# Kernel optimization log

Hardware: AMD Instinct MI355X
Metric: run time of the kernel (lower is better)

Reference implementation:

```python
import jax, jax.numpy as jnp
import numpy as np

LN_ZERO = -100000000000.0
F_, D_, C_, V_ = 250000, 4, 2, 250000
E_ = F_ * D_
CD_ = C_ ** D_


def setup_inputs() -> dict:
    key = jax.random.key(0)
    k1, k2, k3 = jax.random.split(key, 3)
    # each factor has exactly D_ incident edges, one per variable slot
    edge_f = np.repeat(np.arange(E_ // D_ * 0 + F_ * 0 + F_)[:F_], D_)  # [E]
    pos = np.tile(np.arange(D_), F_)  # variable slot of each edge within its factor
    edge_v = np.asarray(jax.random.randint(k3, (E_,), 0, V_))
    # digit of each flat factor state along each axis: digits[k, s] in [0, C)
    state = np.arange(CD_)
    digits = (state[None, :] // (C_ ** (D_ - 1 - np.arange(D_)))[:, None]) % C_  # [D, CD]
    s_p = digits[pos]  # [E, CD]: the edge's own variable state within each factor state
    # permutation indices into the broadcast-first layout [E, C, C^(D-1)]
    scatter_idx = (np.arange(E_)[:, None] * CD_ + s_p * C_ ** (D_ - 1)).reshape(-1)
    fac_states_to_var = (np.arange(E_)[:, None] * C_ + s_p).reshape(-1)
    return {
        "prv_factorToVar_messages": jax.random.normal(k1, (E_, C_), jnp.float32),
        "factor_potentials": jax.random.normal(k2, (F_,) + (C_,) * D_, jnp.float32),
        "facToVar_edge_idx": jnp.asarray(np.stack([edge_f, edge_v]), jnp.int32),
        "facStates_to_varIdx": jnp.asarray(fac_states_to_var, jnp.int32),
        "varToFactorMsg_scatter_indices": jnp.asarray(scatter_idx, jnp.int32),
        "factor_potential_masks": jnp.zeros((F_,) + (C_,) * D_, jnp.int32),
        "factorToVar_messages_masks": jnp.zeros((E_, C_), bool),
        "varToFactor_messages_masks": jnp.zeros((E_, C_), bool),
        "var_beliefs_masks": jnp.zeros((V_, C_), bool),
    }


def _mask_clamp(x, mask):
    return jnp.maximum(jnp.where(mask, LN_ZERO, x), LN_ZERO)


def reference(prv_factorToVar_messages, factor_potentials, facToVar_edge_idx,
              facStates_to_varIdx, varToFactorMsg_scatter_indices,
              factor_potential_masks, factorToVar_messages_masks,
              varToFactor_messages_masks, var_beliefs_masks):
    E, C = prv_factorToVar_messages.shape
    F = factor_potentials.shape[0]
    V = var_beliefs_masks.shape[0]
    D = factor_potentials.ndim - 1
    edge_f, edge_v = facToVar_edge_idx[0], facToVar_edge_idx[1]

    def beliefs(msgs):
        vb = _mask_clamp(jax.ops.segment_sum(msgs, edge_v, num_segments=V), var_beliefs_masks)
        v2f = _mask_clamp(vb[edge_v] - msgs, varToFactor_messages_masks)
        # expanded[e, s] = v2f[e, s_p]; source is broadcast layout [E, C, C^(D-1)]
        expanded = v2f.reshape(-1)[varToFactorMsg_scatter_indices // (C ** (D - 1))]
        expanded = expanded.reshape((E,) + (C,) * D)
        fb = jax.ops.segment_sum(expanded.reshape(E, -1), edge_f, num_segments=F)
        fb = fb.reshape(factor_potentials.shape) + factor_potentials
        fb = jnp.maximum(jnp.where(factor_potential_masks == 1, LN_ZERO, fb), LN_ZERO)
        return vb, v2f, expanded, fb

    prv_vb, prv_v2f, exp_prv_v2f, prv_fb = beliefs(prv_factorToVar_messages)

    # new factor->var messages: max-marginalize (mode='map')
    nfv = prv_fb[edge_f] - exp_prv_v2f
    nfv = nfv - jnp.max(nfv)
    flat = nfv.reshape(-1)
    seg = jnp.where(facStates_to_varIdx >= 0, facStates_to_varIdx, E * C)  # invalid -> dropped slot
    new_f2v = jax.ops.segment_max(flat, seg, num_segments=E * C + 1)[:-1].reshape(E, C)
    # normalization: logsumexp over all dims except dim 0 (here just the state axis)
    new_f2v = new_f2v - jax.nn.logsumexp(new_f2v, axis=1, keepdims=True)
    new_f2v = _mask_clamp(new_f2v, factorToVar_messages_masks)

    vb, v2f, _, fb = beliefs(new_f2v)

    damping = 0.0
    f2v = _mask_clamp(damping * prv_factorToVar_messages + (1.0 - damping) * new_f2v,
                      factorToVar_messages_masks)
    return (f2v, vb, fb)
```

## Files before the change

kernel.cpp:

```cpp
#include <hip/hip_runtime.h>
#include <hip/hip_fp16.h>
#include <math.h>
#include <string.h>

#define LN_ZERO (-100000000000.0f)

constexpr int F_ = 250000;
constexpr int V_ = 250000;
constexpr int E_ = 1000000;

constexpr int NBLK  = 256;
constexpr int PARTS = 256;
constexpr int BINS  = 977;
constexpr int CAP   = 30;
constexpr int SLICE = 3908;
constexpr int OVF_B = 1024;
constexpr int NWAVE = 16;
constexpr int SBUCK = PARTS * CAP;
static_assert(PARTS * BINS >= V_, "");
static_assert((size_t)NBLK * SLICE >= E_, "");
static_assert(SLICE % 4 == 0, "");
static_assert(CAP <= 64, "segment items must fit one wave");
static_assert((size_t)NBLK * PARTS * CAP * 8 <= (size_t)F_ * 16 * 4, "buckets fit in out_fb");

static __device__ inline unsigned pack_h2(float x, float y) {
    __half2 h = __floats2half2_rn(x, y);
    unsigned u; memcpy(&u, &h, 4); return u;
}
static __device__ inline float2 unpack_h2(unsigned u) {
    __half2 h; memcpy(&h, &u, 4); return __half22float2(h);
}

__global__ __launch_bounds__(1024)
void k_ms1(const int* __restrict__ edge_v,
           const float2* __restrict__ msgs,
           const int4* __restrict__ potmask4,
           unsigned short* __restrict__ potbits,
           uint2* __restrict__ buckets,
           int* __restrict__ counts,
           uint2* __restrict__ ovf,
           int* __restrict__ ovf_counts) {
    __shared__ uint2 sbuck[SBUCK];
    __shared__ int cur[PARTS];
    __shared__ int ovf_cur;
    int b = blockIdx.x, tid = threadIdx.x;
    if (tid < PARTS) cur[tid] = 0;
    if (tid == 0) ovf_cur = 0;
    __syncthreads();

    int f = b * 1024 + tid;
    if (f < F_) {
        unsigned int bits = 0;
#pragma unroll
        for (int j = 0; j < 4; ++j) {
            int4 pm = potmask4[4 * f + j];
            bits |= (pm.x == 1 ? 1u : 0u) << (4 * j + 0);
            bits |= (pm.y == 1 ? 1u : 0u) << (4 * j + 1);
            bits |= (pm.z == 1 ? 1u : 0u) << (4 * j + 2);
            bits |= (pm.w == 1 ? 1u : 0u) << (4 * j + 3);
        }
        potbits[f] = (unsigned short)bits;
    }

    int ebase = b * SLICE;
    int eend = min(ebase + SLICE, E_);
    for (int e = ebase + tid; e < eend; e += 1024) {
        int v = edge_v[e];
        int p = v / BINS;
        float2 m = msgs[e];
        unsigned payload = pack_h2(m.x, m.y);
        int pos = atomicAdd(&cur[p], 1);
        if (pos < CAP) {
            sbuck[p * CAP + pos] = make_uint2((unsigned)(v - p * BINS), payload);
        } else {
            int op = atomicAdd(&ovf_cur, 1);
            if (op < OVF_B)
                ovf[(size_t)b * OVF_B + op] = make_uint2((unsigned)v, payload);
        }
    }
    __syncthreads();
    uint2* gb = buckets + (size_t)b * SBUCK;
    for (int j = tid; j < SBUCK; j += 1024) {
        int p = j / CAP;
        int i = j - p * CAP;
        if (i < min(cur[p], CAP)) gb[j] = sbuck[j];
    }
    if (tid < PARTS) counts[tid * NBLK + b] = min(cur[tid], CAP);
    if (tid == 0) ovf_counts[b] = min(ovf_cur, OVF_B);
}

__global__ __launch_bounds__(1024)
void k_acc1(const uint2* __restrict__ buckets,
            const int* __restrict__ counts,
            const uint2* __restrict__ ovf,
            const int* __restrict__ ovf_counts,
            const unsigned short* __restrict__ vb_mask2,
            __half2* __restrict__ accP) {
    __shared__ float2 acc[BINS];
    __shared__ int ls_cnt[NBLK];
    __shared__ int ovfc[NBLK];
    int p = blockIdx.x, tid = threadIdx.x;
    int vbase = p * BINS;
    int nb = min(BINS, V_ - vbase);

    for (int j = tid; j < BINS; j += 1024) acc[j] = make_float2(0.f, 0.f);
    if (tid < NBLK) { ls_cnt[tid] = counts[p * NBLK + tid]; ovfc[tid] = ovf_counts[tid]; }
    __syncthreads();

    int wave = tid >> 6, lane = tid & 63;
    for (int b = wave; b < NBLK; b += NWAVE) {
        int n = ls_cnt[b];
        if (lane < n) {
            uint2 pr = buckets[((size_t)b * PARTS + p) * CAP + lane];
            float2 mv = unpack_h2(pr.y);
            atomicAdd(&acc[pr.x].x, mv.x);
            atomicAdd(&acc[pr.x].y, mv.y);
        }
    }
    for (int b = wave; b < NBLK; b += NWAVE) {
        int n = ovfc[b];
        for (int i = lane; i < n; i += 64) {
            uint2 pr = ovf[(size_t)b * OVF_B + i];
            int vl = (int)pr.x - vbase;
            if ((unsigned)vl < (unsigned)nb) {
                float2 mv = unpack_h2(pr.y);
                atomicAdd(&acc[vl].x, mv.x);
                atomicAdd(&acc[vl].y, mv.y);
            }
        }
    }
    __syncthreads();
    for (int j = tid; j < nb; j += 1024) {
        int v = vbase + j;
        unsigned short vbm = vb_mask2[v];
        float b0 = fmaxf((vbm & 0xff) ? LN_ZERO : acc[j].x, LN_ZERO);
        float b1 = fmaxf((vbm >> 8)   ? LN_ZERO : acc[j].y, LN_ZERO);
        accP[v] = __floats2half2_rn(b0, b1);
    }
}

__global__ __launch_bounds__(1024)
void k_fm_ms2(const float2* __restrict__ msgs,
              const int* __restrict__ edge_v,
              const __half2* __restrict__ accP,
              const float4* __restrict__ pot4,
              const unsigned short* __restrict__ potbits,
              const unsigned short* __restrict__ f2v_mask2,
              const unsigned short* __restrict__ v2f_mask2,
              float2* __restrict__ out_f2v,
              uint2* __restrict__ buckets,
              int* __restrict__ counts,
              uint2* __restrict__ ovf,
              int* __restrict__ ovf_counts) {
    __shared__ uint2 sbuck[SBUCK];
    __shared__ int cur[PARTS];
    __shared__ int ovf_cur;
    int b = blockIdx.x, tid = threadIdx.x;
    if (tid < PARTS) cur[tid] = 0;
    if (tid == 0) ovf_cur = 0;
    __syncthreads();

    int ebase = b * SLICE;
    int eend = min(ebase + SLICE, E_);
    for (int e = ebase + tid; e < eend; e += 1024) {
        int d = e & 3;
        int v = edge_v[e];

        float2 s = __half22float2(accP[v]);
        float2 m = msgs[e];
        unsigned short vm = v2f_mask2[e];
        float wx = fmaxf((vm & 0xff) ? LN_ZERO : (s.x - m.x), LN_ZERO);
        float wy = fmaxf((vm >> 8)   ? LN_ZERO : (s.y - m.y), LN_ZERO);

        float w0x = __shfl(wx, 0, 4), w0y = __shfl(wy, 0, 4);
        float w1x = __shfl(wx, 1, 4), w1y = __shfl(wy, 1, 4);
        float w2x = __shfl(wx, 2, 4), w2y = __shfl(wy, 2, 4);
        float w3x = __shfl(wx, 3, 4), w3y = __shfl(wy, 3, 4);

        float4 p = pot4[e];
        unsigned int pb = potbits[e >> 2] >> (4 * d);
        float A = ((d >> 1) ? w0y : w0x) + ((d & 1) ? w1y : w1x);
        float fb0 = p.x + A + w2x + w3x;
        float fb1 = p.y + A + w2x + w3y;
        float fb2 = p.z + A + w2y + w3x;
        float fb3 = p.w + A + w2y + w3y;
        fb0 = fmaxf((pb & 1u) ? LN_ZERO : fb0, LN_ZERO);
        fb1 = fmaxf((pb & 2u) ? LN_ZERO : fb1, LN_ZERO);
        fb2 = fmaxf((pb & 4u) ? LN_ZERO : fb2, LN_ZERO);
        fb3 = fmaxf((pb & 8u) ? LN_ZERO : fb3, LN_ZERO);

        float mk2_0 = fmaxf(fb0, fb1);
        float mk2_1 = fmaxf(fb2, fb3);
        float mk3_0 = fmaxf(fb0, fb2);
        float mk3_1 = fmaxf(fb1, fb3);
        float mloc  = fmaxf(mk2_0, mk2_1);

#pragma unroll
        for (int off = 1; off < 4; off <<= 1) {
            mk2_0 = fmaxf(mk2_0, __shfl_xor(mk2_0, off, 4));
            mk2_1 = fmaxf(mk2_1, __shfl_xor(mk2_1, off, 4));
            mk3_0 = fmaxf(mk3_0, __shfl_xor(mk3_0, off, 4));
            mk3_1 = fmaxf(mk3_1, __shfl_xor(mk3_1, off, 4));
        }
        float ml0 = __shfl(mloc, 0, 4);
        float ml1 = __shfl(mloc, 1, 4);
        float ml2 = __shfl(mloc, 2, 4);
        float ml3 = __shfl(mloc, 3, 4);

        float mm0, mm1;
        if (d == 0)      { mm0 = fmaxf(ml0, ml1); mm1 = fmaxf(ml2, ml3); }
        else if (d == 1) { mm0 = fmaxf(ml0, ml2); mm1 = fmaxf(ml1, ml3); }
        else if (d == 2) { mm0 = mk2_0;           mm1 = mk2_1; }
        else             { mm0 = mk3_0;           mm1 = mk3_1; }

        float raw0 = mm0 - wx;
        float raw1 = mm1 - wy;
        float mx = fmaxf(raw0, raw1);
        float lse = mx + logf(expf(raw0 - mx) + expf(raw1 - mx));
        unsigned short fm = f2v_mask2[e];
        float o0 = fmaxf((fm & 0xff) ? LN_ZERO : (raw0 - lse), LN_ZERO);
        float o1 = fmaxf((fm >> 8)   ? LN_ZERO : (raw1 - lse), LN_ZERO);
        out_f2v[e] = make_float2(o0, o1);

        int pp = v / BINS;
        unsigned payload = pack_h2(o0, o1);
        int pos = atomicAdd(&cur[pp], 1);
        if (pos < CAP) {
            sbuck[pp * CAP + pos] = make_uint2((unsigned)(v - pp * BINS), payload);
        } else {
            int op = atomicAdd(&ovf_cur, 1);
            if (op < OVF_B)
                ovf[(size_t)b * OVF_B + op] = make_uint2((unsigned)v, payload);
        }
    }
    __syncthreads();
    uint2* gb = buckets + (size_t)b * SBUCK;
    for (int j = tid; j < SBUCK; j += 1024) {
        int p = j / CAP;
        int i = j - p * CAP;
        if (i < min(cur[p], CAP)) gb[j] = sbuck[j];
    }
    if (tid < PARTS) counts[tid * NBLK + b] = min(cur[tid], CAP);
    if (tid == 0) ovf_counts[b] = min(ovf_cur, OVF_B);
}

__global__ __launch_bounds__(1024)
void k_acc2(const uint2* __restrict__ buckets,
            const int* __restrict__ counts,
            const uint2* __restrict__ ovf,
            const int* __restrict__ ovf_counts,
            const unsigned short* __restrict__ vb_mask2,
            float2* __restrict__ out_vb,
            __half2* __restrict__ accN) {
    __shared__ float2 acc[BINS];
    __shared__ int ls_cnt[NBLK];
    __shared__ int ovfc[NBLK];
    int p = blockIdx.x, tid = threadIdx.x;
    int vbase = p * BINS;
    int nb = min(BINS, V_ - vbase);

    for (int j = tid; j < BINS; j += 1024) acc[j] = make_float2(0.f, 0.f);
    if (tid < NBLK) { ls_cnt[tid] = counts[p * NBLK + tid]; ovfc[tid] = ovf_counts[tid]; }
    __syncthreads();

    int wave = tid >> 6, lane = tid & 63;
    for (int b = wave; b < NBLK; b += NWAVE) {
        int n = ls_cnt[b];
        if (lane < n) {
            uint2 pr = buckets[((size_t)b * PARTS + p) * CAP + lane];
            float2 mv = unpack_h2(pr.y);
            atomicAdd(&acc[pr.x].x, mv.x);
            atomicAdd(&acc[pr.x].y, mv.y);
        }
    }
    for (int b = wave; b < NBLK; b += NWAVE) {
        int n = ovfc[b];
        for (int i = lane; i < n; i += 64) {
            uint2 pr = ovf[(size_t)b * OVF_B + i];
            int vl = (int)pr.x - vbase;
            if ((unsigned)vl < (unsigned)nb) {
                float2 mv = unpack_h2(pr.y);
                atomicAdd(&acc[vl].x, mv.x);
                atomicAdd(&acc[vl].y, mv.y);
            }
        }
    }
    __syncthreads();
    for (int j = tid; j < nb; j += 1024) {
        int v = vbase + j;
        unsigned short vbm = vb_mask2[v];
        float b0 = fmaxf((vbm & 0xff) ? LN_ZERO : acc[j].x, LN_ZERO);
        float b1 = fmaxf((vbm >> 8)   ? LN_ZERO : acc[j].y, LN_ZERO);
        out_vb[v] = make_float2(b0, b1);
        accN[v] = __floats2half2_rn(b0, b1);
    }
}

__global__ void k_factor_beliefs(const float2* __restrict__ new_f2v,
                                 const __half2* __restrict__ accN,
                                 const int* __restrict__ edge_v,
                                 const float4* __restrict__ pot4,
                                 const unsigned short* __restrict__ potbits,
                                 const unsigned short* __restrict__ v2f_mask2,
                                 float4* __restrict__ out_fb4) {
    int e = blockIdx.x * blockDim.x + threadIdx.x;
    if (e >= E_) return;
    int d = e & 3;

    float2 b = __half22float2(accN[edge_v[e]]);
    float2 g = new_f2v[e];
    unsigned short vm = v2f_mask2[e];
    float wx = fmaxf((vm & 0xff) ? LN_ZERO : (b.x - g.x), LN_ZERO);
    float wy = fmaxf((vm >> 8)   ? LN_ZERO : (b.y - g.y), LN_ZERO);

    float w0x = __shfl(wx, 0, 4), w0y = __shfl(wy, 0, 4);
    float w1x = __shfl(wx, 1, 4), w1y = __shfl(wy, 1, 4);
    float w2x = __shfl(wx, 2, 4), w2y = __shfl(wy, 2, 4);
    float w3x = __shfl(wx, 3, 4), w3y = __shfl(wy, 3, 4);

    float4 p = pot4[e];
    unsigned int pb = potbits[e >> 2] >> (4 * d);
    float A = ((d >> 1) ? w0y : w0x) + ((d & 1) ? w1y : w1x);
    float o0 = fmaxf((pb & 1u) ? LN_ZERO : (p.x + A + w2x + w3x), LN_ZERO);
    float o1 = fmaxf((pb & 2u) ? LN_ZERO : (p.y + A + w2x + w3y), LN_ZERO);
    float o2 = fmaxf((pb & 4u) ? LN_ZERO : (p.z + A + w2y + w3x), LN_ZERO);
    float o3 = fmaxf((pb & 8u) ? LN_ZERO : (p.w + A + w2y + w3y), LN_ZERO);
    out_fb4[e] = make_float4(o0, o1, o2, o3);
}

extern "C" void kernel_launch(void* const* d_in, const int* in_sizes, int n_in,
                              void* d_out, int out_size, void* d_ws, size_t ws_size,
                              hipStream_t stream) {
    const float* msgs     = (const float*)d_in[0];
    const float* pot      = (const float*)d_in[1];
    const int*   edge_idx = (const int*)d_in[2];
    const int*   pot_mask = (const int*)d_in[5];
    const unsigned char* f2v_mask = (const unsigned char*)d_in[6];
    const unsigned char* v2f_mask = (const unsigned char*)d_in[7];
    const unsigned char* vb_mask  = (const unsigned char*)d_in[8];

    const int* edge_v = edge_idx + E_;

    float* out      = (float*)d_out;
    float* out_f2v  = out;
    float* out_vb   = out + (size_t)E_ * 2;
    float* out_fb   = out_vb + (size_t)V_ * 2;

    uint2* buckets = (uint2*)out_fb;

    int* counts = (int*)d_ws;
    int* ovf_counts = counts + NBLK * PARTS;
    uint2* ovf = (uint2*)(ovf_counts + NBLK);
    __half2* accP = (__half2*)(ovf + (size_t)NBLK * OVF_B);
    __half2* accN = accP + V_;
    unsigned short* potbits = (unsigned short*)(accN + V_);

    const int B = 256;
    dim3 gE((E_ + B - 1) / B);

    k_ms1<<<NBLK, 1024, 0, stream>>>(edge_v, (const float2*)msgs,
                                     (const int4*)pot_mask, potbits,
                                     buckets, counts, ovf, ovf_counts);
    k_acc1<<<PARTS, 1024, 0, stream>>>(buckets, counts, ovf, ovf_counts,
                                       (const unsigned short*)vb_mask, accP);

    k_fm_ms2<<<NBLK, 1024, 0, stream>>>((const float2*)msgs, edge_v, accP,
                                        (const float4*)pot, potbits,
                                        (const unsigned short*)f2v_mask,
                                        (const unsigned short*)v2f_mask,
                                        (float2*)out_f2v,
                                        buckets, counts, ovf, ovf_counts);

    k_acc2<<<PARTS, 1024, 0, stream>>>(buckets, counts, ovf, ovf_counts,
                                       (const unsigned short*)vb_mask,
                                       (float2*)out_vb, accN);

    k_factor_beliefs<<<gE, B, 0, stream>>>((const float2*)out_f2v, accN, edge_v,
                                           (const float4*)pot, potbits,
                                           (const unsigned short*)v2f_mask,
                                           (float4*)out_fb);
}
```

Before: 71.12 us.

## Double block/partition counts, split bucket payload arrays, pack four segments per wave

Doubles the number of edge slices and vertex partitions (512 each) and shrinks bucket capacity, so that two blocks can fit per CU. Bucket entries are split into separate 4-byte payload and 2-byte local-index arrays to cut memory traffic. The accumulate kernels process four 16-entry segments per wave instead of one segment per wave. Smaller capacity raises the chance of overflow-path use, and the overflow scan is now done by more blocks.

```diff
diff --git a/kernel.cpp b/kernel.cpp
--- a/kernel.cpp
+++ b/kernel.cpp
@@ -9,19 +9,19 @@
 constexpr int V_ = 250000;
 constexpr int E_ = 1000000;
 
-constexpr int NBLK  = 256;
-constexpr int PARTS = 256;
-constexpr int BINS  = 977;
-constexpr int CAP   = 30;
-constexpr int SLICE = 3908;
+constexpr int NBLK  = 512;
+constexpr int PARTS = 512;
+constexpr int BINS  = 489;
+constexpr int CAP   = 10;
+constexpr int SLICE = 1956;
 constexpr int OVF_B = 1024;
 constexpr int NWAVE = 16;
 constexpr int SBUCK = PARTS * CAP;
 static_assert(PARTS * BINS >= V_, "");
 static_assert((size_t)NBLK * SLICE >= E_, "");
 static_assert(SLICE % 4 == 0, "");
-static_assert(CAP <= 64, "segment items must fit one wave");
-static_assert((size_t)NBLK * PARTS * CAP * 8 <= (size_t)F_ * 16 * 4, "buckets fit in out_fb");
+static_assert(CAP <= 16, "4 segments per wave iteration needs CAP<=16");
+static_assert((size_t)NBLK * SBUCK * 6 <= (size_t)F_ * 16 * 4, "buckets fit in out_fb");
 
 static __device__ inline unsigned pack_h2(float x, float y) {
     __half2 h = __floats2half2_rn(x, y);
@@ -31,16 +31,18 @@
     __half2 h; memcpy(&h, &u, 4); return __half22float2(h);
 }
 
-__global__ __launch_bounds__(1024)
+__global__ __launch_bounds__(1024, 8)
 void k_ms1(const int* __restrict__ edge_v,
            const float2* __restrict__ msgs,
            const int4* __restrict__ potmask4,
            unsigned short* __restrict__ potbits,
-           uint2* __restrict__ buckets,
+           unsigned* __restrict__ pay,
+           unsigned short* __restrict__ vl,
            int* __restrict__ counts,
            uint2* __restrict__ ovf,
            int* __restrict__ ovf_counts) {
-    __shared__ uint2 sbuck[SBUCK];
+    __shared__ unsigned s_pay[SBUCK];
+    __shared__ unsigned short s_vl[SBUCK];
     __shared__ int cur[PARTS];
     __shared__ int ovf_cur;
     int b = blockIdx.x, tid = threadIdx.x;
@@ -71,7 +73,8 @@
         unsigned payload = pack_h2(m.x, m.y);
         int pos = atomicAdd(&cur[p], 1);
         if (pos < CAP) {
-            sbuck[p * CAP + pos] = make_uint2((unsigned)(v - p * BINS), payload);
+            s_pay[p * CAP + pos] = payload;
+            s_vl[p * CAP + pos] = (unsigned short)(v - p * BINS);
         } else {
             int op = atomicAdd(&ovf_cur, 1);
             if (op < OVF_B)
@@ -79,18 +82,19 @@
         }
     }
     __syncthreads();
-    uint2* gb = buckets + (size_t)b * SBUCK;
+    size_t gbase = (size_t)b * SBUCK;
     for (int j = tid; j < SBUCK; j += 1024) {
         int p = j / CAP;
         int i = j - p * CAP;
-        if (i < min(cur[p], CAP)) gb[j] = sbuck[j];
+        if (i < min(cur[p], CAP)) { pay[gbase + j] = s_pay[j]; vl[gbase + j] = s_vl[j]; }
     }
     if (tid < PARTS) counts[tid * NBLK + b] = min(cur[tid], CAP);
     if (tid == 0) ovf_counts[b] = min(ovf_cur, OVF_B);
 }
 
-__global__ __launch_bounds__(1024)
-void k_acc1(const uint2* __restrict__ buckets,
+__global__ __launch_bounds__(1024, 8)
+void k_acc1(const unsigned* __restrict__ pay,
+            const unsigned short* __restrict__ vl,
             const int* __restrict__ counts,
             const uint2* __restrict__ ovf,
             const int* __restrict__ ovf_counts,
@@ -104,28 +108,34 @@
     int nb = min(BINS, V_ - vbase);
 
     for (int j = tid; j < BINS; j += 1024) acc[j] = make_float2(0.f, 0.f);
-    if (tid < NBLK) { ls_cnt[tid] = counts[p * NBLK + tid]; ovfc[tid] = ovf_counts[tid]; }
+    for (int j = tid; j < NBLK; j += 1024) {
+        ls_cnt[j] = counts[p * NBLK + j];
+        ovfc[j] = ovf_counts[j];
+    }
     __syncthreads();
 
     int wave = tid >> 6, lane = tid & 63;
-    for (int b = wave; b < NBLK; b += NWAVE) {
-        int n = ls_cnt[b];
-        if (lane < n) {
-            uint2 pr = buckets[((size_t)b * PARTS + p) * CAP + lane];
-            float2 mv = unpack_h2(pr.y);
-            atomicAdd(&acc[pr.x].x, mv.x);
-            atomicAdd(&acc[pr.x].y, mv.y);
-        }
-    }
-    for (int b = wave; b < NBLK; b += NWAVE) {
-        int n = ovfc[b];
+    for (int s4 = wave * 4; s4 < NBLK; s4 += NWAVE * 4) {
+        int seg = s4 + (lane >> 4);
+        int idx = lane & 15;
+        int n = ls_cnt[seg];
+        if (idx < n) {
+            size_t base = ((size_t)seg * PARTS + p) * CAP + idx;
+            float2 mv = unpack_h2(pay[base]);
+            int j = vl[base];
+            atomicAdd(&acc[j].x, mv.x);
+            atomicAdd(&acc[j].y, mv.y);
+        }
+    }
+    for (int s = wave; s < NBLK; s += NWAVE) {
+        int n = ovfc[s];
         for (int i = lane; i < n; i += 64) {
-            uint2 pr = ovf[(size_t)b * OVF_B + i];
-            int vl = (int)pr.x - vbase;
-            if ((unsigned)vl < (unsigned)nb) {
+            uint2 pr = ovf[(size_t)s * OVF_B + i];
+            int j = (int)pr.x - vbase;
+            if ((unsigned)j < (unsigned)nb) {
                 float2 mv = unpack_h2(pr.y);
-                atomicAdd(&acc[vl].x, mv.x);
-                atomicAdd(&acc[vl].y, mv.y);
+                atomicAdd(&acc[j].x, mv.x);
+                atomicAdd(&acc[j].y, mv.y);
             }
         }
     }
@@ -139,7 +149,7 @@
     }
 }
 
-__global__ __launch_bounds__(1024)
+__global__ __launch_bounds__(1024, 8)
 void k_fm_ms2(const float2* __restrict__ msgs,
               const int* __restrict__ edge_v,
               const __half2* __restrict__ accP,
@@ -148,11 +158,13 @@
               const unsigned short* __restrict__ f2v_mask2,
               const unsigned short* __restrict__ v2f_mask2,
               float2* __restrict__ out_f2v,
-              uint2* __restrict__ buckets,
+              unsigned* __restrict__ pay,
+              unsigned short* __restrict__ vl,
               int* __restrict__ counts,
               uint2* __restrict__ ovf,
               int* __restrict__ ovf_counts) {
-    __shared__ uint2 sbuck[SBUCK];
+    __shared__ unsigned s_pay[SBUCK];
+    __shared__ unsigned short s_vl[SBUCK];
     __shared__ int cur[PARTS];
     __shared__ int ovf_cur;
     int b = blockIdx.x, tid = threadIdx.x;
@@ -226,7 +238,8 @@
         unsigned payload = pack_h2(o0, o1);
         int pos = atomicAdd(&cur[pp], 1);
         if (pos < CAP) {
-            sbuck[pp * CAP + pos] = make_uint2((unsigned)(v - pp * BINS), payload);
+            s_pay[pp * CAP + pos] = payload;
+            s_vl[pp * CAP + pos] = (unsigned short)(v - pp * BINS);
         } else {
             int op = atomicAdd(&ovf_cur, 1);
             if (op < OVF_B)
@@ -234,18 +247,19 @@
         }
     }
     __syncthreads();
-    uint2* gb = buckets + (size_t)b * SBUCK;
+    size_t gbase = (size_t)b * SBUCK;
     for (int j = tid; j < SBUCK; j += 1024) {
         int p = j / CAP;
         int i = j - p * CAP;
-        if (i < min(cur[p], CAP)) gb[j] = sbuck[j];
+        if (i < min(cur[p], CAP)) { pay[gbase + j] = s_pay[j]; vl[gbase + j] = s_vl[j]; }
     }
     if (tid < PARTS) counts[tid * NBLK + b] = min(cur[tid], CAP);
     if (tid == 0) ovf_counts[b] = min(ovf_cur, OVF_B);
 }
 
-__global__ __launch_bounds__(1024)
-void k_acc2(const uint2* __restrict__ buckets,
+__global__ __launch_bounds__(1024, 8)
+void k_acc2(const unsigned* __restrict__ pay,
+            const unsigned short* __restrict__ vl,
             const int* __restrict__ counts,
             const uint2* __restrict__ ovf,
             const int* __restrict__ ovf_counts,
@@ -260,28 +274,34 @@
     int nb = min(BINS, V_ - vbase);
 
     for (int j = tid; j < BINS; j += 1024) acc[j] = make_float2(0.f, 0.f);
-    if (tid < NBLK) { ls_cnt[tid] = counts[p * NBLK + tid]; ovfc[tid] = ovf_counts[tid]; }
+    for (int j = tid; j < NBLK; j += 1024) {
+        ls_cnt[j] = counts[p * NBLK + j];
+        ovfc[j] = ovf_counts[j];
+    }
     __syncthreads();
 
     int wave = tid >> 6, lane = tid & 63;
-    for (int b = wave; b < NBLK; b += NWAVE) {
-        int n = ls_cnt[b];
-        if (lane < n) {
-            uint2 pr = buckets[((size_t)b * PARTS + p) * CAP + lane];
-            float2 mv = unpack_h2(pr.y);
-            atomicAdd(&acc[pr.x].x, mv.x);
-            atomicAdd(&acc[pr.x].y, mv.y);
-        }
-    }
-    for (int b = wave; b < NBLK; b += NWAVE) {
-        int n = ovfc[b];
+    for (int s4 = wave * 4; s4 < NBLK; s4 += NWAVE * 4) {
+        int seg = s4 + (lane >> 4);
+        int idx = lane & 15;
+        int n = ls_cnt[seg];
+        if (idx < n) {
+            size_t base = ((size_t)seg * PARTS + p) * CAP + idx;
+            float2 mv = unpack_h2(pay[base]);
+            int j = vl[base];
+            atomicAdd(&acc[j].x, mv.x);
+            atomicAdd(&acc[j].y, mv.y);
+        }
+    }
+    for (int s = wave; s < NBLK; s += NWAVE) {
+        int n = ovfc[s];
         for (int i = lane; i < n; i += 64) {
-            uint2 pr = ovf[(size_t)b * OVF_B + i];
-            int vl = (int)pr.x - vbase;
-            if ((unsigned)vl < (unsigned)nb) {
+            uint2 pr = ovf[(size_t)s * OVF_B + i];
+            int j = (int)pr.x - vbase;
+            if ((unsigned)j < (unsigned)nb) {
                 float2 mv = unpack_h2(pr.y);
-                atomicAdd(&acc[vl].x, mv.x);
-                atomicAdd(&acc[vl].y, mv.y);
+                atomicAdd(&acc[j].x, mv.x);
+                atomicAdd(&acc[j].y, mv.y);
             }
         }
     }
@@ -346,7 +366,8 @@
     float* out_vb   = out + (size_t)E_ * 2;
     float* out_fb   = out_vb + (size_t)V_ * 2;
 
-    uint2* buckets = (uint2*)out_fb;
+    unsigned* pay = (unsigned*)out_fb;
+    unsigned short* vl = (unsigned short*)(pay + (size_t)NBLK * SBUCK);
 
     int* counts = (int*)d_ws;
     int* ovf_counts = counts + NBLK * PARTS;
@@ -360,8 +381,8 @@
 
     k_ms1<<<NBLK, 1024, 0, stream>>>(edge_v, (const float2*)msgs,
                                      (const int4*)pot_mask, potbits,
-                                     buckets, counts, ovf, ovf_counts);
-    k_acc1<<<PARTS, 1024, 0, stream>>>(buckets, counts, ovf, ovf_counts,
+                                     pay, vl, counts, ovf, ovf_counts);
+    k_acc1<<<PARTS, 1024, 0, stream>>>(pay, vl, counts, ovf, ovf_counts,
                                        (const unsigned short*)vb_mask, accP);
 
     k_fm_ms2<<<NBLK, 1024, 0, stream>>>((const float2*)msgs, edge_v, accP,
@@ -369,9 +390,9 @@
                                         (const unsigned short*)f2v_mask,
                                         (const unsigned short*)v2f_mask,
                                         (float2*)out_f2v,
-                                        buckets, counts, ovf, ovf_counts);
-
-    k_acc2<<<PARTS, 1024, 0, stream>>>(buckets, counts, ovf, ovf_counts,
+                                        pay, vl, counts, ovf, ovf_counts);
+
+    k_acc2<<<PARTS, 1024, 0, stream>>>(pay, vl, counts, ovf, ovf_counts,
                                        (const unsigned short*)vb_mask,
                                        (float2*)out_vb, accN);
 
```

Result: slower. 87.77 us (+23.4%).
